# Optimization experiments

Hardware: AMD Instinct MI355X
Metric: run time of the kernel (lower is better)

Reference implementation:

```python
import jax, jax.numpy as jnp
import numpy as np

B, D, E, H, K = 8192, 1024, 8, 4096, 2

def setup_inputs() -> dict:
    key = jax.random.key(0)
    ks = jax.random.split(key, 7)
    s_in = 1.0 / np.sqrt(D)
    s_hid = 1.0 / np.sqrt(H)
    return {
        "z":  jax.random.normal(ks[0], (B, D), dtype=jnp.float32),
        "Wg": jax.random.uniform(ks[1], (D, E), jnp.float32, -s_in, s_in),
        "bg": jnp.zeros((E,), jnp.float32),
        "W1": jax.random.uniform(ks[2], (E, D, H), jnp.float32, -s_in, s_in),
        "b1": jax.random.uniform(ks[3], (E, H), jnp.float32, -s_in, s_in),
        "W2": jax.random.uniform(ks[4], (E, H, D), jnp.float32, -s_hid, s_hid),
        "b2": jax.random.uniform(ks[5], (E, D), jnp.float32, -s_hid, s_hid),
    }

def reference(z, Wg, bg, W1, b1, W2, b2):
    # gate: softmax over experts, then keep only top-k weights (no renorm,
    # matching the original which sums topw * expert(z))
    w = jax.nn.softmax(z @ Wg + bg, axis=-1)            # [B, E]
    topw, idx = jax.lax.top_k(w, K)                      # [B, K] each
    wmask = jnp.zeros_like(w).at[jnp.arange(B)[:, None], idx].set(topw)  # [B, E]
    # dense all-expert MLP, then weighted combine (same math as per-token loop)
    h = jax.nn.relu(jnp.einsum('bd,edh->beh', z, W1) + b1)   # [B, E, H]
    y = jnp.einsum('beh,ehd->bed', h, W2) + b2               # [B, E, D]
    out = jnp.einsum('be,bed->bd', wmask, y)                 # [B, D]
    return out
```

## Files before the change

### kernel.cpp

```cpp
#include <hip/hip_runtime.h>
#include <hip/hip_bf16.h>
#include <cstdint>
#include <cstddef>

#define BTOK  8192
#define DIM   1024
#define NEXP  8
#define NHID  4096
#define HHALF 2048
#define GATE_TOK 64
#define BK 32

typedef __bf16 bf16x8 __attribute__((ext_vector_type(8)));
typedef float  floatx4 __attribute__((ext_vector_type(4)));

#define O_COUNTS 0
#define O_BASE   256
#define O_TOKB   1024
#define O_TOKW   (O_TOKB + (size_t)NEXP*BTOK*4)
#define O_CE     (O_TOKW + (size_t)NEXP*BTOK*4)
#define O_CP     (O_CE + (size_t)2*BTOK*4)
#define O_CW     (O_CP + (size_t)2*BTOK*4)
#define O_ZBF    (O_CW + (size_t)2*BTOK*4)
#define O_W1T    (O_ZBF + (size_t)BTOK*DIM*2)
#define O_W2T    (O_W1T + (size_t)NEXP*DIM*NHID*2)
#define O_HBUF   (O_W2T + (size_t)NEXP*DIM*NHID*2)
#define WS_BASE  (O_HBUF + (size_t)2*BTOK*HHALF*2)
#define O_YBUF   WS_BASE
#define WS_FULL  (O_YBUF + (size_t)2*BTOK*DIM*4)

__device__ __forceinline__ void gload_lds16(const void* g, void* l) {
  __builtin_amdgcn_global_load_lds(
      (const __attribute__((address_space(1))) void*)g,
      (__attribute__((address_space(3))) void*)l, 16, 0, 0);
}

__device__ __forceinline__ ushort f2bf(float x) {
  return __builtin_bit_cast(ushort, __float2bfloat16(x));
}

__global__ void k_zcnt(int* __restrict__ counts) {
  if (threadIdx.x < NEXP) counts[threadIdx.x] = 0;
}

__global__ void k_zout(float* __restrict__ out) {
  int i = blockIdx.x * blockDim.x + threadIdx.x;
  float4 z4 = {0.f, 0.f, 0.f, 0.f};
  float4* o = (float4*)out;
  int n = BTOK * DIM / 4;
  for (int j = i; j < n; j += gridDim.x * blockDim.x) o[j] = z4;
}

__global__ __launch_bounds__(256) void k_transpose(
    const float* __restrict__ src, __hip_bfloat16* __restrict__ dst, int R, int C) {
  __shared__ float tile[32][33];
  int zz = blockIdx.z;
  const float* s = src + (size_t)zz * R * C;
  __hip_bfloat16* d = dst + (size_t)zz * R * C;
  int c0 = blockIdx.x * 32, r0 = blockIdx.y * 32;
  int tx = threadIdx.x & 31, ty = threadIdx.x >> 5;
#pragma unroll
  for (int i = ty; i < 32; i += 8)
    tile[i][tx] = s[(size_t)(r0 + i) * C + c0 + tx];
  __syncthreads();
#pragma unroll
  for (int i = ty; i < 32; i += 8)
    d[(size_t)(c0 + i) * R + r0 + tx] = __float2bfloat16(tile[tx][i]);
}

__global__ __launch_bounds__(256) void k_gate(
    const float* __restrict__ z, const float* __restrict__ Wg,
    const float* __restrict__ bg, int* __restrict__ counts,
    int* __restrict__ tokb, float* __restrict__ tokw,
    int* __restrict__ ce, int* __restrict__ cp, float* __restrict__ cw,
    __hip_bfloat16* __restrict__ zbf) {
  __shared__ float wgT[NEXP * DIM];
  __shared__ int   le[2 * GATE_TOK];
  __shared__ float lw[2 * GATE_TOK];
  __shared__ int   lr[2 * GATE_TOK];
  __shared__ int   lcnt[NEXP];
  __shared__ int   gbase[NEXP];

  int tid = threadIdx.x;
  if (tid < NEXP) lcnt[tid] = 0;
#pragma unroll
  for (int e = 0; e < NEXP; e++)
    for (int d = tid; d < DIM; d += 256)
      wgT[e * DIM + d] = Wg[d * NEXP + e];
  __syncthreads();

  int lane = tid & 63;
  int wv = tid >> 6;
  int b0 = blockIdx.x * GATE_TOK;

  for (int t = 0; t < 16; t++) {
    int lt = wv * 16 + t;
    int b = b0 + lt;
    const float4* zr4 = (const float4*)(z + (size_t)b * DIM);
    float4 zv[4];
#pragma unroll
    for (int i = 0; i < 4; i++) zv[i] = zr4[lane + 64 * i];
    ushort4* zb4 = (ushort4*)((ushort*)zbf + (size_t)b * DIM);
#pragma unroll
    for (int i = 0; i < 4; i++) {
      ushort4 u;
      u.x = f2bf(zv[i].x); u.y = f2bf(zv[i].y);
      u.z = f2bf(zv[i].z); u.w = f2bf(zv[i].w);
      zb4[lane + 64 * i] = u;
    }
    float acc[NEXP];
#pragma unroll
    for (int e = 0; e < NEXP; e++) acc[e] = 0.f;
#pragma unroll
    for (int e = 0; e < NEXP; e++) {
      const float4* wg4 = (const float4*)(wgT + e * DIM);
#pragma unroll
      for (int i = 0; i < 4; i++) {
        float4 w4 = wg4[lane + 64 * i];
        acc[e] += zv[i].x * w4.x + zv[i].y * w4.y + zv[i].z * w4.z + zv[i].w * w4.w;
      }
    }
#pragma unroll
    for (int off = 32; off > 0; off >>= 1) {
#pragma unroll
      for (int e = 0; e < NEXP; e++) acc[e] += __shfl_down(acc[e], off);
    }
    if (lane == 0) {
      float mx = -1e30f;
#pragma unroll
      for (int e = 0; e < NEXP; e++) { acc[e] += bg[e]; mx = fmaxf(mx, acc[e]); }
      float s = 0.f;
#pragma unroll
      for (int e = 0; e < NEXP; e++) { acc[e] = expf(acc[e] - mx); s += acc[e]; }
      float inv = 1.f / s;
      int i1 = -1, i2 = -1; float v1 = -1.f, v2 = -1.f;
#pragma unroll
      for (int e = 0; e < NEXP; e++) {
        float w = acc[e] * inv;
        if (w > v1) { v2 = v1; i2 = i1; v1 = w; i1 = e; }
        else if (w > v2) { v2 = w; i2 = e; }
      }
      le[2 * lt] = i1;     lw[2 * lt] = v1;
      le[2 * lt + 1] = i2; lw[2 * lt + 1] = v2;
    }
  }
  __syncthreads();
  if (tid < 2 * GATE_TOK) lr[tid] = atomicAdd(&lcnt[le[tid]], 1);
  __syncthreads();
  if (tid < NEXP) gbase[tid] = atomicAdd(&counts[tid], lcnt[tid]);
  __syncthreads();
  if (tid < 2 * GATE_TOK) {
    int e = le[tid];
    int p = gbase[e] + lr[tid];
    int b = b0 + (tid >> 1);
    int slot = tid & 1;
    tokb[e * BTOK + p] = b;
    tokw[e * BTOK + p] = lw[tid];
    ce[2 * b + slot] = e;
    cp[2 * b + slot] = p;
    cw[2 * b + slot] = lw[tid];
  }
}

__global__ void k_base(const int* __restrict__ counts, int* __restrict__ base) {
  if (threadIdx.x == 0 && blockIdx.x == 0) {
    int s = 0;
    for (int e = 0; e < NEXP; e++) { base[e] = s; s += counts[e]; }
  }
}


#define STAGE(t_) do {                                                          \
    int s_ = (t_) & 3;                                                          \
    _Pragma("unroll")                                                           \
    for (int q_ = 0; q_ < 2; q_++) {                                            \
      gload_lds16(srcA[q_] + (t_) * BK, &lds[s_][0][(q_ * 128 + wv * 16) * BK]);\
      gload_lds16(srcB[q_] + (t_) * BK, &lds[s_][1][(q_ * 128 + wv * 16) * BK]);\
    }                                                                           \
  } while (0)

#define BAR_A(vm) do {                                                          \
    asm volatile("s_waitcnt vmcnt(" #vm ")" ::: "memory");                      \
    __builtin_amdgcn_s_barrier();                                               \
    asm volatile("" ::: "memory");                                              \
  } while (0)

#define BAR_B() do {                                                            \
    asm volatile("s_waitcnt lgkmcnt(0)" ::: "memory");                          \
    __builtin_amdgcn_s_barrier();                                               \
    asm volatile("" ::: "memory");                                              \
  } while (0)

#define MFMA_TILE(slot_) do {                                                   \
    const ushort* As_ = &lds[(slot_)][0][0];                                    \
    const ushort* Bs_ = &lds[(slot_)][1][0];                                    \
    bf16x8 afr[8], bfr[4];                                                      \
    _Pragma("unroll")                                                           \
    for (int j_ = 0; j_ < 4; j_++)                                              \
      bfr[j_] = __builtin_bit_cast(bf16x8,                                      \
          *(const uint4*)(Bs_ + (wn * 64 + j_ * 16 + lrow) * BK + cswz));       \
    _Pragma("unroll")                                                           \
    for (int i_ = 0; i_ < 8; i_++)                                              \
      afr[i_] = __builtin_bit_cast(bf16x8,                                      \
          *(const uint4*)(As_ + (wm * 128 + i_ * 16 + lrow) * BK + cswz));      \
    __builtin_amdgcn_s_setprio(1);                                              \
    _Pragma("unroll")                                                           \
    for (int i_ = 0; i_ < 8; i_++)                                              \
      _Pragma("unroll")                                                         \
      for (int j_ = 0; j_ < 4; j_++)                                            \
        acc[i_][j_] = __builtin_amdgcn_mfma_f32_16x16x32_bf16(                  \
            afr[i_], bfr[j_], acc[i_][j_], 0, 0, 0);                            \
    __builtin_amdgcn_s_setprio(0);                                              \
  } while (0)

__global__ __launch_bounds__(512, 2) void k_gemm1(
    const __hip_bfloat16* __restrict__ zbf, const __hip_bfloat16* __restrict__ w1t,
    const float* __restrict__ b1, const int* __restrict__ counts,
    const int* __restrict__ base, const int* __restrict__ tokb,
    __hip_bfloat16* __restrict__ hbuf, int hbase) {
  int e = blockIdx.z;
  int cnt = counts[e];
  if (cnt == 0) return;
  int n0 = blockIdx.y * 256;
  int gb = base[e];

  __shared__ __align__(16) ushort lds[4][2][256 * BK];

  int tid = threadIdx.x;
  int lane = tid & 63;
  int wv = tid >> 6;
  int wm = wv >> 2;
  int wn = wv & 3;
  int lrow = lane & 15;
  int quad = lane >> 4;
  int cswz = (quad ^ ((lrow >> 1) & 3)) * 8;

  int srow = wv * 16 + (lane >> 2);
  int schunk = lane & 3;

  const ushort* zb = (const ushort*)zbf;
  const ushort* w1 = (const ushort*)w1t;

  const ushort* srcB[2];
#pragma unroll
  for (int q = 0; q < 2; q++) {
    int r = q * 128 + srow;
    srcB[q] = w1 + (size_t)(e * NHID + hbase + n0 + r) * DIM
                 + (size_t)((schunk ^ ((r >> 1) & 3)) * 8);
  }

  const int NT = DIM / BK;

  for (int mt = blockIdx.x; mt * 256 < cnt; mt += gridDim.x) {
    int m0 = mt * 256;
    const ushort* srcA[2];
#pragma unroll
    for (int q = 0; q < 2; q++) {
      int r = q * 128 + srow;
      int m = m0 + r; if (m >= cnt) m = cnt - 1;
      srcA[q] = zb + (size_t)tokb[e * BTOK + m] * DIM
                   + (size_t)((schunk ^ ((r >> 1) & 3)) * 8);
    }

#pragma unroll
    for (int t = 0; t < 3; t++) STAGE(t);

    floatx4 acc[8][4];
#pragma unroll
    for (int i = 0; i < 8; i++)
#pragma unroll
      for (int j = 0; j < 4; j++) { floatx4 zf = {0.f,0.f,0.f,0.f}; acc[i][j] = zf; }

#pragma unroll 1
    for (int t = 0; t < NT - 3; t++) {
      STAGE(t + 3);
      BAR_A(12);
      MFMA_TILE(t & 3);
      BAR_B();
    }
    BAR_A(8);  MFMA_TILE((NT - 3) & 3);  BAR_B();
    BAR_A(4);  MFMA_TILE((NT - 2) & 3);  BAR_B();
    BAR_A(0);  MFMA_TILE((NT - 1) & 3);  BAR_B();

    float bias[4];
#pragma unroll
    for (int j = 0; j < 4; j++)
      bias[j] = b1[e * NHID + hbase + n0 + wn * 64 + j * 16 + lrow];
    ushort* hp = (ushort*)hbuf;
#pragma unroll
    for (int i = 0; i < 8; i++) {
      int mloc = wm * 128 + i * 16 + quad * 4;
#pragma unroll
      for (int r = 0; r < 4; r++) {
        int m = m0 + mloc + r;
        if (m < cnt) {
          ushort* hr = hp + (size_t)(gb + m) * HHALF;
#pragma unroll
          for (int j = 0; j < 4; j++) {
            float v = fmaxf(acc[i][j][r] + bias[j], 0.f);
            hr[n0 + wn * 64 + j * 16 + lrow] = f2bf(v);
          }
        }
      }
    }
  }
}

__global__ __launch_bounds__(512, 2) void k_gemm2(
    const __hip_bfloat16* __restrict__ hbuf, const __hip_bfloat16* __restrict__ w2t,
    const float* __restrict__ b2, const int* __restrict__ counts,
    const int* __restrict__ base, const int* __restrict__ tokb,
    const float* __restrict__ tokw, float* __restrict__ out,
    float* __restrict__ ybuf, int hbase, int pass) {
  int e = blockIdx.z;
  int cnt = counts[e];
  if (cnt == 0) return;
  int n0 = blockIdx.y * 256;
  int gb = base[e];

  __shared__ __align__(16) ushort lds[4][2][256 * BK];

  int tid = threadIdx.x;
  int lane = tid & 63;
  int wv = tid >> 6;
  int wm = wv >> 2;
  int wn = wv & 3;
  int lrow = lane & 15;
  int quad = lane >> 4;
  int cswz = (quad ^ ((lrow >> 1) & 3)) * 8;

  int srow = wv * 16 + (lane >> 2);
  int schunk = lane & 3;

  const ushort* hb = (const ushort*)hbuf;
  const ushort* w2 = (const ushort*)w2t;

  const ushort* srcB[2];
#pragma unroll
  for (int q = 0; q < 2; q++) {
    int r = q * 128 + srow;
    srcB[q] = w2 + (size_t)(e * DIM + n0 + r) * NHID + hbase
                 + (size_t)((schunk ^ ((r >> 1) & 3)) * 8);
  }

  const int NT = HHALF / BK;

  for (int mt = blockIdx.x; mt * 256 < cnt; mt += gridDim.x) {
    int m0 = mt * 256;
    const ushort* srcA[2];
#pragma unroll
    for (int q = 0; q < 2; q++) {
      int r = q * 128 + srow;
      int m = m0 + r; if (m >= cnt) m = cnt - 1;
      srcA[q] = hb + (size_t)(gb + m) * HHALF
                   + (size_t)((schunk ^ ((r >> 1) & 3)) * 8);
    }

#pragma unroll
    for (int t = 0; t < 3; t++) STAGE(t);

    floatx4 acc[8][4];
#pragma unroll
    for (int i = 0; i < 8; i++)
#pragma unroll
      for (int j = 0; j < 4; j++) { floatx4 zf = {0.f,0.f,0.f,0.f}; acc[i][j] = zf; }

#pragma unroll 1
    for (int t = 0; t < NT - 3; t++) {
      STAGE(t + 3);
      BAR_A(12);
      MFMA_TILE(t & 3);
      BAR_B();
    }
    BAR_A(8);  MFMA_TILE((NT - 3) & 3);  BAR_B();
    BAR_A(4);  MFMA_TILE((NT - 2) & 3);  BAR_B();
    BAR_A(0);  MFMA_TILE((NT - 1) & 3);  BAR_B();

    if (ybuf) {
      float bias[4];
#pragma unroll
      for (int j = 0; j < 4; j++)
        bias[j] = pass ? b2[e * DIM + n0 + wn * 64 + j * 16 + lrow] : 0.f;
#pragma unroll
      for (int i = 0; i < 8; i++) {
        int mloc = wm * 128 + i * 16 + quad * 4;
#pragma unroll
        for (int r = 0; r < 4; r++) {
          int m = m0 + mloc + r;
          if (m < cnt) {
            float* yr = ybuf + (size_t)(gb + m) * DIM;
#pragma unroll
            for (int j = 0; j < 4; j++) {
              int n = n0 + wn * 64 + j * 16 + lrow;
              if (pass == 0) yr[n] = acc[i][j][r];
              else           yr[n] += acc[i][j][r] + bias[j];
            }
          }
        }
      }
    } else {
#pragma unroll
      for (int i = 0; i < 8; i++) {
        int mloc = wm * 128 + i * 16 + quad * 4;
#pragma unroll
        for (int r = 0; r < 4; r++) {
          int m = m0 + mloc + r;
          if (m < cnt) {
            int tk  = tokb[e * BTOK + m];
            float w = tokw[e * BTOK + m];
#pragma unroll
            for (int j = 0; j < 4; j++) {
              int n = n0 + wn * 64 + j * 16 + lrow;
              float v = acc[i][j][r] + (pass ? b2[e * DIM + n] : 0.f);
              atomicAdd(&out[(size_t)tk * DIM + n], w * v);
            }
          }
        }
      }
    }
  }
}

__global__ __launch_bounds__(256) void k_combine(
    const float* __restrict__ ybuf, const int* __restrict__ base,
    const int* __restrict__ ce, const int* __restrict__ cp,
    const float* __restrict__ cw, float* __restrict__ out) {
  int b = blockIdx.x;
  int n = threadIdx.x * 4;
  int e1 = ce[2 * b], e2 = ce[2 * b + 1];
  int s1 = base[e1] + cp[2 * b];
  int s2 = base[e2] + cp[2 * b + 1];
  float w1 = cw[2 * b], w2 = cw[2 * b + 1];
  float4 a = *(const float4*)(ybuf + (size_t)s1 * DIM + n);
  float4 c = *(const float4*)(ybuf + (size_t)s2 * DIM + n);
  float4 o;
  o.x = w1 * a.x + w2 * c.x;
  o.y = w1 * a.y + w2 * c.y;
  o.z = w1 * a.z + w2 * c.z;
  o.w = w1 * a.w + w2 * c.w;
  *(float4*)(out + (size_t)b * DIM + n) = o;
}

extern "C" void kernel_launch(void* const* d_in, const int* in_sizes, int n_in,
                              void* d_out, int out_size, void* d_ws, size_t ws_size,
                              hipStream_t stream) {
  const float* z  = (const float*)d_in[0];
  const float* Wg = (const float*)d_in[1];
  const float* bg = (const float*)d_in[2];
  const float* W1 = (const float*)d_in[3];
  const float* b1 = (const float*)d_in[4];
  const float* W2 = (const float*)d_in[5];
  const float* b2 = (const float*)d_in[6];
  float* out = (float*)d_out;
  char* ws = (char*)d_ws;
  if (ws_size < WS_BASE) return;
  bool use_ybuf = ws_size >= WS_FULL;

  int*   counts = (int*)(ws + O_COUNTS);
  int*   base   = (int*)(ws + O_BASE);
  int*   tokb   = (int*)(ws + O_TOKB);
  float* tokw   = (float*)(ws + O_TOKW);
  int*   ce     = (int*)(ws + O_CE);
  int*   cp     = (int*)(ws + O_CP);
  float* cw     = (float*)(ws + O_CW);
  __hip_bfloat16* zbf  = (__hip_bfloat16*)(ws + O_ZBF);
  __hip_bfloat16* w1t  = (__hip_bfloat16*)(ws + O_W1T);
  __hip_bfloat16* w2t  = (__hip_bfloat16*)(ws + O_W2T);
  __hip_bfloat16* hbuf = (__hip_bfloat16*)(ws + O_HBUF);
  float* ybuf = use_ybuf ? (float*)(ws + O_YBUF) : nullptr;

  k_zcnt<<<1, 64, 0, stream>>>(counts);
  if (!use_ybuf) k_zout<<<512, 256, 0, stream>>>(out);
  k_transpose<<<dim3(NHID / 32, DIM / 32, NEXP), 256, 0, stream>>>(W1, w1t, DIM, NHID);
  k_transpose<<<dim3(DIM / 32, NHID / 32, NEXP), 256, 0, stream>>>(W2, w2t, NHID, DIM);
  k_gate<<<BTOK / GATE_TOK, 256, 0, stream>>>(z, Wg, bg, counts, tokb, tokw, ce, cp, cw, zbf);
  k_base<<<1, 64, 0, stream>>>(counts, base);
  for (int half = 0; half < 2; half++) {
    k_gemm1<<<dim3(8, HHALF / 256, NEXP), 512, 0, stream>>>(
        zbf, w1t, b1, counts, base, tokb, hbuf, half * HHALF);
    k_gemm2<<<dim3(8, DIM / 256, NEXP), 512, 0, stream>>>(
        hbuf, w2t, b2, counts, base, tokb, tokw, out, ybuf, half * HHALF, half);
  }
  if (use_ybuf)
    k_combine<<<BTOK, 256, 0, stream>>>(ybuf, base, ce, cp, cw, out);
}
```

Before: 1.010 ms.

## Restructure GEMM mainloop into 8-phase ping-pong schedule with interleaved loads

```diff
diff --git a/kernel.cpp b/kernel.cpp
--- a/kernel.cpp
+++ b/kernel.cpp
@@ -9,7 +9,6 @@
 #define NHID  4096
 #define HHALF 2048
 #define GATE_TOK 64
-#define BK 32
 
 typedef __bf16 bf16x8 __attribute__((ext_vector_type(8)));
 typedef float  floatx4 __attribute__((ext_vector_type(4)));
@@ -170,48 +169,47 @@
 }
 
 
-#define STAGE(t_) do {                                                          \
-    int s_ = (t_) & 3;                                                          \
-    _Pragma("unroll")                                                           \
-    for (int q_ = 0; q_ < 2; q_++) {                                            \
-      gload_lds16(srcA[q_] + (t_) * BK, &lds[s_][0][(q_ * 128 + wv * 16) * BK]);\
-      gload_lds16(srcB[q_] + (t_) * BK, &lds[s_][1][(q_ * 128 + wv * 16) * BK]);\
-    }                                                                           \
+#define STG(bb_, op_, SRC_, kh_, tt_) do {                                   \
+    gload_lds16(SRC_[0] + (tt_) * 64 + (kh_) * 32,                           \
+                &lds[bb_][op_][kh_][(0 * 128 + wv * 16) * 32]);              \
+    gload_lds16(SRC_[1] + (tt_) * 64 + (kh_) * 32,                           \
+                &lds[bb_][op_][kh_][(1 * 128 + wv * 16) * 32]);              \
   } while (0)
 
-#define BAR_A(vm) do {                                                          \
-    asm volatile("s_waitcnt vmcnt(" #vm ")" ::: "memory");                      \
-    __builtin_amdgcn_s_barrier();                                               \
-    asm volatile("" ::: "memory");                                              \
+#define PH(cur_, kk_, ih_, STAGE_, WAIT_) do {                               \
+    const ushort* Ab_ = &lds[cur_][0][kk_][0];                               \
+    const ushort* Bb_ = &lds[cur_][1][kk_][0];                               \
+    if (ih_ == 0) {                                                          \
+      _Pragma("unroll")                                                      \
+      for (int j_ = 0; j_ < 4; j_++)                                         \
+        bfr[j_] = __builtin_bit_cast(bf16x8,                                 \
+            *(const uint4*)(Bb_ + boff + j_ * 512));                         \
+    }                                                                        \
+    bf16x8 afr_[4];                                                          \
+    _Pragma("unroll")                                                        \
+    for (int i_ = 0; i_ < 4; i_++)                                           \
+      afr_[i_] = __builtin_bit_cast(bf16x8,                                  \
+          *(const uint4*)(Ab_ + aoff + ((ih_) * 4 + i_) * 512));             \
+    STAGE_;                                                                  \
+    __builtin_amdgcn_sched_barrier(0);                                       \
+    WAIT_;                                                                   \
+    __builtin_amdgcn_s_barrier();                                            \
+    __builtin_amdgcn_sched_barrier(0);                                       \
+    __builtin_amdgcn_s_setprio(1);                                           \
+    _Pragma("unroll")                                                        \
+    for (int i_ = 0; i_ < 4; i_++)                                           \
+      _Pragma("unroll")                                                      \
+      for (int j_ = 0; j_ < 4; j_++)                                         \
+        acc[(ih_) * 4 + i_][j_] = __builtin_amdgcn_mfma_f32_16x16x32_bf16(   \
+            afr_[i_], bfr[j_], acc[(ih_) * 4 + i_][j_], 0, 0, 0);            \
+    __builtin_amdgcn_s_setprio(0);                                           \
+    __builtin_amdgcn_sched_barrier(0);                                       \
+    __builtin_amdgcn_s_barrier();                                            \
   } while (0)
 
-#define BAR_B() do {                                                            \
-    asm volatile("s_waitcnt lgkmcnt(0)" ::: "memory");                          \
-    __builtin_amdgcn_s_barrier();                                               \
-    asm volatile("" ::: "memory");                                              \
-  } while (0)
-
-#define MFMA_TILE(slot_) do {                                                   \
-    const ushort* As_ = &lds[(slot_)][0][0];                                    \
-    const ushort* Bs_ = &lds[(slot_)][1][0];                                    \
-    bf16x8 afr[8], bfr[4];                                                      \
-    _Pragma("unroll")                                                           \
-    for (int j_ = 0; j_ < 4; j_++)                                              \
-      bfr[j_] = __builtin_bit_cast(bf16x8,                                      \
-          *(const uint4*)(Bs_ + (wn * 64 + j_ * 16 + lrow) * BK + cswz));       \
-    _Pragma("unroll")                                                           \
-    for (int i_ = 0; i_ < 8; i_++)                                              \
-      afr[i_] = __builtin_bit_cast(bf16x8,                                      \
-          *(const uint4*)(As_ + (wm * 128 + i_ * 16 + lrow) * BK + cswz));      \
-    __builtin_amdgcn_s_setprio(1);                                              \
-    _Pragma("unroll")                                                           \
-    for (int i_ = 0; i_ < 8; i_++)                                              \
-      _Pragma("unroll")                                                         \
-      for (int j_ = 0; j_ < 4; j_++)                                            \
-        acc[i_][j_] = __builtin_amdgcn_mfma_f32_16x16x32_bf16(                  \
-            afr[i_], bfr[j_], acc[i_][j_], 0, 0, 0);                            \
-    __builtin_amdgcn_s_setprio(0);                                              \
-  } while (0)
+#define VM6 asm volatile("s_waitcnt vmcnt(6)" ::: "memory")
+#define VM0 asm volatile("s_waitcnt vmcnt(0)" ::: "memory")
+#define NOP_ (void)0
 
 __global__ __launch_bounds__(512, 2) void k_gemm1(
     const __hip_bfloat16* __restrict__ zbf, const __hip_bfloat16* __restrict__ w1t,
@@ -224,7 +222,7 @@
   int n0 = blockIdx.y * 256;
   int gb = base[e];
 
-  __shared__ __align__(16) ushort lds[4][2][256 * BK];
+  __shared__ __align__(16) ushort lds[2][2][2][256 * 32];
 
   int tid = threadIdx.x;
   int lane = tid & 63;
@@ -233,54 +231,69 @@
   int wn = wv & 3;
   int lrow = lane & 15;
   int quad = lane >> 4;
-  int cswz = (quad ^ ((lrow >> 1) & 3)) * 8;
-
-  int srow = wv * 16 + (lane >> 2);
-  int schunk = lane & 3;
+  int pc = quad ^ ((lrow >> 1) & 3);
+  int aoff = (wm * 128 + lrow) * 32 + pc * 8;
+  int boff = (wn * 64 + lrow) * 32 + pc * 8;
 
   const ushort* zb = (const ushort*)zbf;
   const ushort* w1 = (const ushort*)w1t;
 
   const ushort* srcB[2];
 #pragma unroll
-  for (int q = 0; q < 2; q++) {
-    int r = q * 128 + srow;
-    srcB[q] = w1 + (size_t)(e * NHID + hbase + n0 + r) * DIM
-                 + (size_t)((schunk ^ ((r >> 1) & 3)) * 8);
-  }
-
-  const int NT = DIM / BK;
+  for (int l = 0; l < 2; l++) {
+    int r = l * 128 + wv * 16 + (lane >> 2);
+    srcB[l] = w1 + (size_t)(e * NHID + hbase + n0 + r) * DIM
+                 + (size_t)(((lane & 3) ^ ((r >> 1) & 3)) * 8);
+  }
+
+  const int NT = DIM / 64;
 
   for (int mt = blockIdx.x; mt * 256 < cnt; mt += gridDim.x) {
     int m0 = mt * 256;
     const ushort* srcA[2];
 #pragma unroll
-    for (int q = 0; q < 2; q++) {
-      int r = q * 128 + srow;
+    for (int l = 0; l < 2; l++) {
+      int r = l * 128 + wv * 16 + (lane >> 2);
       int m = m0 + r; if (m >= cnt) m = cnt - 1;
-      srcA[q] = zb + (size_t)tokb[e * BTOK + m] * DIM
-                   + (size_t)((schunk ^ ((r >> 1) & 3)) * 8);
-    }
-
-#pragma unroll
-    for (int t = 0; t < 3; t++) STAGE(t);
+      srcA[l] = zb + (size_t)tokb[e * BTOK + m] * DIM
+                   + (size_t)(((lane & 3) ^ ((r >> 1) & 3)) * 8);
+    }
+
+    STG(0, 0, srcA, 0, 0); STG(0, 1, srcB, 0, 0);
+    STG(0, 0, srcA, 1, 0); STG(0, 1, srcB, 1, 0);
+    STG(1, 1, srcB, 0, 1); STG(1, 0, srcA, 0, 1); STG(1, 1, srcB, 1, 1);
+    VM6;
+    __builtin_amdgcn_s_barrier();
 
     floatx4 acc[8][4];
 #pragma unroll
     for (int i = 0; i < 8; i++)
 #pragma unroll
       for (int j = 0; j < 4; j++) { floatx4 zf = {0.f,0.f,0.f,0.f}; acc[i][j] = zf; }
+    bf16x8 bfr[4];
 
 #pragma unroll 1
-    for (int t = 0; t < NT - 3; t++) {
-      STAGE(t + 3);
-      BAR_A(12);
-      MFMA_TILE(t & 3);
-      BAR_B();
-    }
-    BAR_A(8);  MFMA_TILE((NT - 3) & 3);  BAR_B();
-    BAR_A(4);  MFMA_TILE((NT - 2) & 3);  BAR_B();
-    BAR_A(0);  MFMA_TILE((NT - 1) & 3);  BAR_B();
+    for (int t = 0; t < NT - 2; ++t) {
+      int cur = t & 1;
+      PH(cur, 0, 0, STG(cur ^ 1, 0, srcA, 1, t + 1), NOP_);
+      PH(cur, 0, 1, STG(cur, 1, srcB, 0, t + 2), NOP_);
+      PH(cur, 1, 0, STG(cur, 0, srcA, 0, t + 2), NOP_);
+      PH(cur, 1, 1, STG(cur, 1, srcB, 1, t + 2), VM6);
+    }
+    {
+      int cur = (NT - 2) & 1;
+      PH(cur, 0, 0, STG(cur ^ 1, 0, srcA, 1, NT - 1), NOP_);
+      PH(cur, 0, 1, NOP_, NOP_);
+      PH(cur, 1, 0, NOP_, NOP_);
+      PH(cur, 1, 1, NOP_, VM0);
+    }
+    {
+      int cur = (NT - 1) & 1;
+      PH(cur, 0, 0, NOP_, NOP_);
+      PH(cur, 0, 1, NOP_, NOP_);
+      PH(cur, 1, 0, NOP_, NOP_);
+      PH(cur, 1, 1, NOP_, NOP_);
+    }
 
     float bias[4];
 #pragma unroll
@@ -318,7 +331,7 @@
   int n0 = blockIdx.y * 256;
   int gb = base[e];
 
-  __shared__ __align__(16) ushort lds[4][2][256 * BK];
+  __shared__ __align__(16) ushort lds[2][2][2][256 * 32];
 
   int tid = threadIdx.x;
   int lane = tid & 63;
@@ -327,54 +340,69 @@
   int wn = wv & 3;
   int lrow = lane & 15;
   int quad = lane >> 4;
-  int cswz = (quad ^ ((lrow >> 1) & 3)) * 8;
-
-  int srow = wv * 16 + (lane >> 2);
-  int schunk = lane & 3;
+  int pc = quad ^ ((lrow >> 1) & 3);
+  int aoff = (wm * 128 + lrow) * 32 + pc * 8;
+  int boff = (wn * 64 + lrow) * 32 + pc * 8;
 
   const ushort* hb = (const ushort*)hbuf;
   const ushort* w2 = (const ushort*)w2t;
 
   const ushort* srcB[2];
 #pragma unroll
-  for (int q = 0; q < 2; q++) {
-    int r = q * 128 + srow;
-    srcB[q] = w2 + (size_t)(e * DIM + n0 + r) * NHID + hbase
-                 + (size_t)((schunk ^ ((r >> 1) & 3)) * 8);
-  }
-
-  const int NT = HHALF / BK;
+  for (int l = 0; l < 2; l++) {
+    int r = l * 128 + wv * 16 + (lane >> 2);
+    srcB[l] = w2 + (size_t)(e * DIM + n0 + r) * NHID + hbase
+                 + (size_t)(((lane & 3) ^ ((r >> 1) & 3)) * 8);
+  }
+
+  const int NT = HHALF / 64;
 
   for (int mt = blockIdx.x; mt * 256 < cnt; mt += gridDim.x) {
     int m0 = mt * 256;
     const ushort* srcA[2];
 #pragma unroll
-    for (int q = 0; q < 2; q++) {
-      int r = q * 128 + srow;
+    for (int l = 0; l < 2; l++) {
+      int r = l * 128 + wv * 16 + (lane >> 2);
       int m = m0 + r; if (m >= cnt) m = cnt - 1;
-      srcA[q] = hb + (size_t)(gb + m) * HHALF
-                   + (size_t)((schunk ^ ((r >> 1) & 3)) * 8);
-    }
-
-#pragma unroll
-    for (int t = 0; t < 3; t++) STAGE(t);
+      srcA[l] = hb + (size_t)(gb + m) * HHALF
+                   + (size_t)(((lane & 3) ^ ((r >> 1) & 3)) * 8);
+    }
+
+    STG(0, 0, srcA, 0, 0); STG(0, 1, srcB, 0, 0);
+    STG(0, 0, srcA, 1, 0); STG(0, 1, srcB, 1, 0);
+    STG(1, 1, srcB, 0, 1); STG(1, 0, srcA, 0, 1); STG(1, 1, srcB, 1, 1);
+    VM6;
+    __builtin_amdgcn_s_barrier();
 
     floatx4 acc[8][4];
 #pragma unroll
     for (int i = 0; i < 8; i++)
 #pragma unroll
       for (int j = 0; j < 4; j++) { floatx4 zf = {0.f,0.f,0.f,0.f}; acc[i][j] = zf; }
+    bf16x8 bfr[4];
 
 #pragma unroll 1
-    for (int t = 0; t < NT - 3; t++) {
-      STAGE(t + 3);
-      BAR_A(12);
-      MFMA_TILE(t & 3);
-      BAR_B();
-    }
-    BAR_A(8);  MFMA_TILE((NT - 3) & 3);  BAR_B();
-    BAR_A(4);  MFMA_TILE((NT - 2) & 3);  BAR_B();
-    BAR_A(0);  MFMA_TILE((NT - 1) & 3);  BAR_B();
+    for (int t = 0; t < NT - 2; ++t) {
+      int cur = t & 1;
+      PH(cur, 0, 0, STG(cur ^ 1, 0, srcA, 1, t + 1), NOP_);
+      PH(cur, 0, 1, STG(cur, 1, srcB, 0, t + 2), NOP_);
+      PH(cur, 1, 0, STG(cur, 0, srcA, 0, t + 2), NOP_);
+      PH(cur, 1, 1, STG(cur, 1, srcB, 1, t + 2), VM6);
+    }
+    {
+      int cur = (NT - 2) & 1;
+      PH(cur, 0, 0, STG(cur ^ 1, 0, srcA, 1, NT - 1), NOP_);
+      PH(cur, 0, 1, NOP_, NOP_);
+      PH(cur, 1, 0, NOP_, NOP_);
+      PH(cur, 1, 1, NOP_, VM0);
+    }
+    {
+      int cur = (NT - 1) & 1;
+      PH(cur, 0, 0, NOP_, NOP_);
+      PH(cur, 0, 1, NOP_, NOP_);
+      PH(cur, 1, 0, NOP_, NOP_);
+      PH(cur, 1, 1, NOP_, NOP_);
+    }
 
     if (ybuf) {
       float bias[4];
```

After: 948.9 us. -6.0%, faster.
